# Kernel optimization log

Hardware: AMD Instinct MI355X
Metric: run time of the kernel (lower is better)

## Reference

```python
import jax, jax.numpy as jnp
import numpy as np

B, C, N = 2, 29, 8192
S, K = 1024, 16  # npoint, nsample
D = C + 3


def fps(xyz_t, npoint):
    # xyz_t: [B, N, 3] -> indices [B, npoint] (furthest point sampling, starts at idx 0)
    b, n, _ = xyz_t.shape

    def step(carry, _):
        dists, farthest = carry  # [B,N], [B]
        centroid = jnp.take_along_axis(xyz_t, farthest[:, None, None], axis=1)  # [B,1,3]
        d = jnp.sum((xyz_t - centroid) ** 2, axis=-1)  # [B,N]
        dists = jnp.minimum(dists, d)
        nxt = jnp.argmax(dists, axis=-1)
        return (dists, nxt), farthest

    init = (jnp.full((b, n), 1e10, xyz_t.dtype), jnp.zeros((b,), jnp.int32))
    _, idx = jax.lax.scan(step, init, None, length=npoint)
    return jnp.transpose(idx)  # [B, npoint]


def knn_self(pts, k):
    # pts: [B, S, 3] -> k nearest neighbor indices within the same set, [B, S, k]
    sq = jnp.sum(pts * pts, axis=-1)
    d2 = sq[:, :, None] + sq[:, None, :] - 2.0 * jnp.einsum('bic,bjc->bij', pts, pts)
    _, idx = jax.lax.top_k(-d2, k)
    return idx


def group(arr, idx):
    # arr: [B, C, N], idx: [B, S, K] -> [B, C, S, K]
    return jax.vmap(lambda a, i: a[:, i])(arr, idx)


def squeeze_2x2(x):
    # RealNVP alt-order squeeze: [n, c, h, w] -> [n, 4c, h/2, w/2]
    tl = x[:, :, 0::2, 0::2]
    br = x[:, :, 1::2, 1::2]
    tr = x[:, :, 0::2, 1::2]
    bl = x[:, :, 1::2, 0::2]
    return jnp.concatenate([tl, br, tr, bl], axis=1)


def conv2d(x, w):
    return jax.lax.conv_general_dilated(
        x, w, window_strides=(1, 1), padding='VALID',
        dimension_numbers=('NCHW', 'OIHW', 'NCHW'))


def setup_inputs() -> dict:
    key = jax.random.key(0)
    ks = jax.random.split(key, 6)
    return {
        'xyz': jax.random.normal(ks[0], (B, 3, N), jnp.float32),
        'feats': jax.random.normal(ks[1], (B, C, N), jnp.float32),
        'w0': jax.random.normal(ks[2], (64, 2 * D * 4, 3, 3), jnp.float32) * 0.02,
        'w1': jax.random.normal(ks[3], (64, 64, 3, 3), jnp.float32) * 0.02,
        'w2': jax.random.normal(ks[4], (128, 64, 3, 3), jnp.float32) * 0.02,
        'w3': jax.random.normal(ks[5], (128, 128, 2, 2), jnp.float32) * 0.02,
    }


def reference(xyz, feats, w0, w1, w2, w3):
    b, c, n = feats.shape
    xyz_t = jnp.transpose(xyz, (0, 2, 1))  # [B,N,3]
    fps_idx = fps(xyz_t, S)  # [B,S]
    new_xyz = jnp.take_along_axis(xyz, fps_idx[:, None, :], axis=2)  # [B,3,S]
    new_xyz_t = jnp.transpose(new_xyz, (0, 2, 1))  # [B,S,3]
    idx = knn_self(new_xyz_t, K)  # [B,S,K], values in [0,S)

    pos_grouped = group(new_xyz, idx)  # [B,3,S,K]
    feats_grouped = group(feats, idx)  # [B,C,S,K] (indices < S, as in original)
    pos_diff = pos_grouped - new_xyz[:, :, :, None]
    fg = jnp.concatenate([pos_diff, feats_grouped], axis=1)  # [B,D,S,K]

    # pairwise outer-product features; second half ([fg;1] x [fg;1] upper block) is all ones
    outer = jnp.einsum('bdsi,bdsj->bdsij', fg, fg)  # [B,D,S,K,K]
    mat = jnp.concatenate([outer, jnp.ones_like(outer)], axis=1)  # [B,2D,S,K,K]
    mat = jnp.transpose(mat, (0, 2, 1, 3, 4)).reshape(b * S, 2 * D, K, K)
    mat = squeeze_2x2(mat)  # [B*S, 8D, K/2, K/2]

    for w in (w0, w1, w2, w3):  # use_bn=False -> Identity bns; spatial 8->6->4->2->1
        mat = jax.nn.relu(conv2d(mat, w))

    new_points = jnp.transpose(mat.reshape(b, S, -1), (0, 2, 1))  # [B,128,S]
    return new_xyz, new_points, fps_idx
```

## Files before the change

kernel.cpp:

```cpp
#include <hip/hip_runtime.h>
#include <hip/hip_bf16.h>

#pragma clang fp contract(off)

#define NPTS 8192
#define NS   1024
#define NB   2
#define NC   29
#define NK   16


__global__ __launch_bounds__(256) void prep_kernel(
    const float* __restrict__ w0, const float* __restrict__ w1,
    const float* __restrict__ w2, const float* __restrict__ w3,
    float* __restrict__ w0t, float* __restrict__ w1t,
    float* __restrict__ w2t, float* __restrict__ w3t,
    float* __restrict__ bias0)
{
    int i = blockIdx.x * 256 + threadIdx.x;
    int n = gridDim.x * 256;
    for (int e = i; e < 73728; e += n) {
        int o = e & 63, r = e >> 6, tap = r % 9, ic2 = r / 9;
        int ic = ((ic2 >> 5) << 6) + (ic2 & 31);
        w0t[e] = w0[(o * 256 + ic) * 9 + tap];
    }
    for (int e = i; e < 36864; e += n) {
        int o = e & 63, r = e >> 6, tap = r % 9, ic = r / 9;
        w1t[e] = w1[(o * 64 + ic) * 9 + tap];
    }
    for (int e = i; e < 73728; e += n) {
        int o = e & 127, r = e >> 7, tap = r % 9, ic = r / 9;
        w2t[e] = w2[(o * 64 + ic) * 9 + tap];
    }
    for (int e = i; e < 65536; e += n) {
        int o = e & 127, r = e >> 7, tap = r & 3, ic = r >> 2;
        w3t[e] = w3[(o * 128 + ic) * 4 + tap];
    }
    if (i < 64) {
        float sum = 0.0f;
        for (int q = 0; q < 4; ++q)
            for (int c = 0; c < 32; ++c)
                for (int t = 0; t < 9; ++t)
                    sum += w0[(i * 256 + q * 64 + 32 + c) * 9 + t];
        bias0[i] = sum;
    }
}

__device__ __forceinline__ float wave_max_nonneg(float x) {
    int v = __float_as_int(x);
    int t;
    t = __builtin_amdgcn_update_dpp(0, v, 0x111, 0xf, 0xf, true);
    v = __float_as_int(fmaxf(__int_as_float(v), __int_as_float(t)));
    t = __builtin_amdgcn_update_dpp(0, v, 0x112, 0xf, 0xf, true);
    v = __float_as_int(fmaxf(__int_as_float(v), __int_as_float(t)));
    t = __builtin_amdgcn_update_dpp(0, v, 0x114, 0xf, 0xf, true);
    v = __float_as_int(fmaxf(__int_as_float(v), __int_as_float(t)));
    t = __builtin_amdgcn_update_dpp(0, v, 0x118, 0xf, 0xf, true);
    v = __float_as_int(fmaxf(__int_as_float(v), __int_as_float(t)));
    t = __builtin_amdgcn_update_dpp(0, v, 0x142, 0xa, 0xf, true);
    v = __float_as_int(fmaxf(__int_as_float(v), __int_as_float(t)));
    t = __builtin_amdgcn_update_dpp(0, v, 0x143, 0xc, 0xf, true);
    v = __float_as_int(fmaxf(__int_as_float(v), __int_as_float(t)));
    return __int_as_float(__builtin_amdgcn_readlane(v, 63));
}

__global__ __launch_bounds__(512, 2) void fps_kernel(
    const float* __restrict__ xyz,
    float* __restrict__ nx_ws, float* __restrict__ out)
{
    int b = blockIdx.x;
    int tid = threadIdx.x;
    const float* X = xyz + b * 3 * NPTS;

    __shared__ float s_xyz[3 * NPTS];
    __shared__ unsigned long long s_key[NS];

    float px[16], py[16], pz[16], dist[16];
#pragma unroll
    for (int i = 0; i < 16; ++i) {
        int gi = i * 512 + tid;
        float x = X[gi], y = X[NPTS + gi], z = X[2 * NPTS + gi];
        px[i] = x; py[i] = y; pz[i] = z;
        dist[i] = 1e10f;
        s_xyz[gi] = x; s_xyz[NPTS + gi] = y; s_xyz[2 * NPTS + gi] = z;
    }
    for (int i = tid; i < NS; i += 512) s_key[i] = 0ull;
    if (tid == 0) s_key[0] = 0xFFFFFFFFull;
    __syncthreads();

    float cx = s_xyz[0], cy = s_xyz[NPTS], cz = s_xyz[2 * NPTS];

    for (int it = 1; it < NS; ++it) {
#pragma unroll
        for (int i = 0; i < 16; ++i)
            asm volatile("" : "+v"(px[i]), "+v"(py[i]), "+v"(pz[i]));
#pragma unroll
        for (int i = 0; i < 16; ++i) {
            float dx = px[i] - cx, dy = py[i] - cy, dz = pz[i] - cz;
            float d = (dx * dx + dy * dy) + dz * dz;
            dist[i] = fminf(dist[i], d);
        }
        float t8[8];
#pragma unroll
        for (int i = 0; i < 8; ++i) t8[i] = fmaxf(dist[2 * i], dist[2 * i + 1]);
        float t4[4];
#pragma unroll
        for (int i = 0; i < 4; ++i) t4[i] = fmaxf(t8[2 * i], t8[2 * i + 1]);
        float bv = fmaxf(fmaxf(t4[0], t4[1]), fmaxf(t4[2], t4[3]));
        float wm = wave_max_nonneg(bv);
        if (bv == wm) {
            int gi = 0;
#pragma unroll
            for (int i = 15; i >= 0; --i)
                if (dist[i] == wm) gi = i * 512 + tid;
            unsigned long long key =
                ((unsigned long long)__float_as_uint(wm) << 32) | (unsigned)(~gi);
            atomicMax(&s_key[it], key);
        }
        __syncthreads();
        int idx = (int)(~(unsigned)s_key[it]);
        cx = s_xyz[idx]; cy = s_xyz[NPTS + idx]; cz = s_xyz[2 * NPTS + idx];
    }

    float* out_fps = out + 268288 + b * NS;
    for (int i = tid; i < NS; i += 512) {
        int j = (int)(~(unsigned)s_key[i]);
        out_fps[i] = (float)j;
        float x = s_xyz[j], y = s_xyz[NPTS + j], z = s_xyz[2 * NPTS + j];
        nx_ws[(b * 3 + 0) * NS + i] = x; out[(b * 3 + 0) * NS + i] = x;
        nx_ws[(b * 3 + 1) * NS + i] = y; out[(b * 3 + 1) * NS + i] = y;
        nx_ws[(b * 3 + 2) * NS + i] = z; out[(b * 3 + 2) * NS + i] = z;
    }
}

__global__ __launch_bounds__(256) void knn_kernel(
    const float* __restrict__ nx_ws, int* __restrict__ knn_ws)
{
    int q = blockIdx.x * 4 + (threadIdx.x >> 6);
    int lane = threadIdx.x & 63;
    int b = q >> 10, s = q & 1023;
    const float* P = nx_ws + b * 3 * NS;
    float qx = P[s], qy = P[NS + s], qz = P[2 * NS + s];
    float sqq = (qx * qx + qy * qy) + qz * qz;
    int base_j = lane * 16;
    float d2[16];
    {
        const float4* x4 = (const float4*)(P + base_j);
        const float4* y4 = (const float4*)(P + NS + base_j);
        const float4* z4 = (const float4*)(P + 2 * NS + base_j);
#pragma unroll
        for (int t = 0; t < 4; ++t) {
            float4 xv = x4[t], yv = y4[t], zv = z4[t];
            float xs[4] = { xv.x, xv.y, xv.z, xv.w };
            float ys[4] = { yv.x, yv.y, yv.z, yv.w };
            float zs[4] = { zv.x, zv.y, zv.z, zv.w };
#pragma unroll
            for (int e = 0; e < 4; ++e) {
                float xj = xs[e], yj = ys[e], zj = zs[e];
                float sqj = (xj * xj + yj * yj) + zj * zj;
                float dot = (qx * xj + qy * yj) + qz * zj;
                d2[t * 4 + e] = (sqq + sqj) - 2.0f * dot;
            }
        }
    }
    for (int r = 0; r < NK; ++r) {
        float lv = 3.0e38f; int li = 0;
#pragma unroll
        for (int i = 0; i < 16; ++i) { if (d2[i] < lv) { lv = d2[i]; li = i; } }
        int gj = base_j + li;
#pragma unroll
        for (int off = 32; off > 0; off >>= 1) {
            float ov = __shfl_xor(lv, off, 64);
            int   oj = __shfl_xor(gj, off, 64);
            if (ov < lv || (ov == lv && oj < gj)) { lv = ov; gj = oj; }
        }
        if (lane == 0) knn_ws[q * NK + r] = gj;
        if ((gj >> 4) == lane) {
            int li2 = gj & 15;
#pragma unroll
            for (int i = 0; i < 16; ++i) if (i == li2) d2[i] = 3.0e38f;
        }
    }
}

template<int GODD>
__device__ __forceinline__ void conv0_accum(
    const float* __restrict__ x0r, const float* __restrict__ wbase, float acc[9])
{
    for (int ic2 = 0; ic2 < 128; ++ic2) {
        const float4* x4 = (const float4*)(x0r + ic2 * 64);
        float rr[32];
#pragma unroll
        for (int j = 0; j < 4; ++j) {
            float4 t0 = x4[j * 2], t1 = x4[j * 2 + 1];
            rr[j*8+0]=t0.x; rr[j*8+1]=t0.y; rr[j*8+2]=t0.z; rr[j*8+3]=t0.w;
            rr[j*8+4]=t1.x; rr[j*8+5]=t1.y; rr[j*8+6]=t1.z; rr[j*8+7]=t1.w;
        }
        float w[9];
#pragma unroll
        for (int t = 0; t < 9; ++t) w[t] = wbase[(ic2 * 9 + t) * 64];
#pragma unroll
        for (int pp = 0; pp < 9; ++pp) {
            const int ly = GODD ? (pp < 3 ? 0 : 1) : (pp < 6 ? 0 : 1);
            const int xx = GODD ? (pp < 3 ? pp + 3 : pp - 3) : (pp < 6 ? pp : pp - 6);
#pragma unroll
            for (int ky = 0; ky < 3; ++ky)
#pragma unroll
                for (int kx = 0; kx < 3; ++kx)
                    acc[pp] = __builtin_fmaf(w[ky * 3 + kx], rr[(ly + ky) * 8 + xx + kx], acc[pp]);
        }
    }
}

__global__ __launch_bounds__(256) void conv_kernel(
    const float* __restrict__ feats, const float* __restrict__ nx_ws,
    const int* __restrict__ knn_ws,
    const float* __restrict__ w0t, const float* __restrict__ bias0,
    const float* __restrict__ w1t, const float* __restrict__ w2t,
    const float* __restrict__ w3t, float* __restrict__ out)
{
    __shared__ float s_fg[512];
    __shared__ int   s_ni[16];
    __shared__ float s_x0[8192];
    __shared__ float s_a1[64 * 36];
    __shared__ float s_a2[64 * 16];
    __shared__ float s_a3[128 * 4];

    int bs = blockIdx.x, b = bs >> 10, s = bs & 1023;
    int tid = threadIdx.x;
    if (tid < 16) s_ni[tid] = knn_ws[bs * NK + tid];
    __syncthreads();
    const float* P = nx_ws + b * 3 * NS;
#pragma unroll
    for (int e = tid; e < 512; e += 256) {
        int d = e >> 4, k = e & 15; int j = s_ni[k];
        float v = (d < 3) ? (P[d * NS + j] - P[d * NS + s])
                          : feats[(b * NC + (d - 3)) * NPTS + j];
        s_fg[e] = v;
    }
    __syncthreads();
    for (int e = tid; e < 8192; e += 256) {
        int ic2 = e >> 6, pos = e & 63, u = pos >> 3, v = pos & 7;
        int q = ic2 >> 5, ch = ic2 & 31;
        int ro = q & 1, co = ((q + 1) >> 1) & 1;
        s_x0[e] = s_fg[ch * 16 + 2 * u + ro] * s_fg[ch * 16 + 2 * v + co];
    }
    __syncthreads();

    int o = tid & 63, g = tid >> 6;
    {
        int r0 = g + (g >> 1);
        float acc[9];
        float bz = bias0[o];
#pragma unroll
        for (int p = 0; p < 9; ++p) acc[p] = bz;
        const float* x0r = s_x0 + r0 * 8;
        const float* wb = w0t + o;
        if (g & 1) conv0_accum<1>(x0r, wb, acc);
        else       conv0_accum<0>(x0r, wb, acc);
#pragma unroll
        for (int pp = 0; pp < 9; ++pp) s_a1[o * 36 + g * 9 + pp] = fmaxf(acc[pp], 0.0f);
    }
    __syncthreads();
    {
        float a[4] = {0, 0, 0, 0};
        const float* wb = w1t + o;
        for (int ic = 0; ic < 64; ++ic) {
            const float2* ar2 = (const float2*)(s_a1 + ic * 36 + g * 6);
            float r[18];
#pragma unroll
            for (int t = 0; t < 9; ++t) { float2 tv = ar2[t]; r[t*2] = tv.x; r[t*2+1] = tv.y; }
            float w[9];
#pragma unroll
            for (int t = 0; t < 9; ++t) w[t] = wb[(ic * 9 + t) * 64];
#pragma unroll
            for (int x = 0; x < 4; ++x)
#pragma unroll
                for (int ky = 0; ky < 3; ++ky)
#pragma unroll
                    for (int kx = 0; kx < 3; ++kx)
                        a[x] = __builtin_fmaf(w[ky * 3 + kx], r[ky * 6 + x + kx], a[x]);
        }
#pragma unroll
        for (int x = 0; x < 4; ++x) s_a2[o * 16 + g * 4 + x] = fmaxf(a[x], 0.0f);
    }
    __syncthreads();
    {
        int o2 = tid & 127, g2 = tid >> 7;
        float a[2] = {0, 0};
        const float* wb = w2t + o2;
        for (int ic = 0; ic < 64; ++ic) {
            const float4* ar4 = (const float4*)(s_a2 + ic * 16 + g2 * 4);
            float r[12];
#pragma unroll
            for (int t = 0; t < 3; ++t) { float4 tv = ar4[t]; r[t*4]=tv.x; r[t*4+1]=tv.y; r[t*4+2]=tv.z; r[t*4+3]=tv.w; }
            float w[9];
#pragma unroll
            for (int t = 0; t < 9; ++t) w[t] = wb[(ic * 9 + t) * 128];
#pragma unroll
            for (int x = 0; x < 2; ++x)
#pragma unroll
                for (int ky = 0; ky < 3; ++ky)
#pragma unroll
                    for (int kx = 0; kx < 3; ++kx)
                        a[x] = __builtin_fmaf(w[ky * 3 + kx], r[ky * 4 + x + kx], a[x]);
        }
#pragma unroll
        for (int x = 0; x < 2; ++x) s_a3[o2 * 4 + g2 * 2 + x] = fmaxf(a[x], 0.0f);
    }
    __syncthreads();
    if (tid < 128) {
        float acc = 0.0f;
        const float* wb = w3t + tid;
        for (int ic = 0; ic < 128; ++ic) {
            float4 av = *(const float4*)(s_a3 + ic * 4);
            float wa = wb[(ic * 4 + 0) * 128];
            float wbv = wb[(ic * 4 + 1) * 128];
            float wc = wb[(ic * 4 + 2) * 128];
            float wd = wb[(ic * 4 + 3) * 128];
            acc = __builtin_fmaf(wa, av.x, acc);
            acc = __builtin_fmaf(wbv, av.y, acc);
            acc = __builtin_fmaf(wc, av.z, acc);
            acc = __builtin_fmaf(wd, av.w, acc);
        }
        out[6144 + (b * 128 + tid) * NS + s] = fmaxf(acc, 0.0f);
    }
}

extern "C" void kernel_launch(void* const* d_in, const int* in_sizes, int n_in,
                              void* d_out, int out_size, void* d_ws, size_t ws_size,
                              hipStream_t stream) {
    const float* xyz   = (const float*)d_in[0];
    const float* feats = (const float*)d_in[1];
    const float* w0    = (const float*)d_in[2];
    const float* w1    = (const float*)d_in[3];
    const float* w2    = (const float*)d_in[4];
    const float* w3    = (const float*)d_in[5];
    float* out = (float*)d_out;

    char* ws = (char*)d_ws;
    float* nx_ws  = (float*)(ws + 8192);
    int*   knn_ws = (int*)(ws + 32768);
    float* w0t    = (float*)(ws + 163840);
    float* bias0  = (float*)(ws + 458752);
    float* w1t    = (float*)(ws + 459008);
    float* w2t    = (float*)(ws + 606464);
    float* w3t    = (float*)(ws + 901376);

    prep_kernel<<<128, 256, 0, stream>>>(w0, w1, w2, w3, w0t, w1t, w2t, w3t, bias0);
    fps_kernel<<<NB, 512, 0, stream>>>(xyz, nx_ws, out);
    knn_kernel<<<(NB * NS) / 4, 256, 0, stream>>>(nx_ws, knn_ws);
    conv_kernel<<<NB * NS, 256, 0, stream>>>(feats, nx_ws, knn_ws, w0t, bias0, w1t, w2t, w3t, out);
}
```

Baseline: 1.402 ms.

## Compute outer-product conv0 inputs on the fly instead of staging in LDS

The 8192-float squeezed outer-product tensor is no longer materialised in shared memory. Each thread now recomputes its input rows from the 512-float grouped features inside the conv0 loop, with one template instance per row group. This cuts LDS from about 45KB to about 13KB and removes a barrier, allowing more resident blocks (launch bounds now request 4 per SM), at the cost of extra multiplies and more unrolled code per thread.

After: 1.431 ms. 2.1% more time.

```diff
diff --git a/kernel.cpp b/kernel.cpp
--- a/kernel.cpp
+++ b/kernel.cpp
@@ -183,36 +183,47 @@
     }
 }
 
-template<int GODD>
+template<int G>
 __device__ __forceinline__ void conv0_accum(
-    const float* __restrict__ x0r, const float* __restrict__ wbase, float acc[9])
-{
-    for (int ic2 = 0; ic2 < 128; ++ic2) {
-        const float4* x4 = (const float4*)(x0r + ic2 * 64);
-        float rr[32];
-#pragma unroll
-        for (int j = 0; j < 4; ++j) {
-            float4 t0 = x4[j * 2], t1 = x4[j * 2 + 1];
-            rr[j*8+0]=t0.x; rr[j*8+1]=t0.y; rr[j*8+2]=t0.z; rr[j*8+3]=t0.w;
-            rr[j*8+4]=t1.x; rr[j*8+5]=t1.y; rr[j*8+6]=t1.z; rr[j*8+7]=t1.w;
-        }
-        float w[9];
-#pragma unroll
-        for (int t = 0; t < 9; ++t) w[t] = wbase[(ic2 * 9 + t) * 64];
-#pragma unroll
-        for (int pp = 0; pp < 9; ++pp) {
-            const int ly = GODD ? (pp < 3 ? 0 : 1) : (pp < 6 ? 0 : 1);
-            const int xx = GODD ? (pp < 3 ? pp + 3 : pp - 3) : (pp < 6 ? pp : pp - 6);
-#pragma unroll
-            for (int ky = 0; ky < 3; ++ky)
-#pragma unroll
-                for (int kx = 0; kx < 3; ++kx)
-                    acc[pp] = __builtin_fmaf(w[ky * 3 + kx], rr[(ly + ky) * 8 + xx + kx], acc[pp]);
-        }
-    }
-}
-
-__global__ __launch_bounds__(256) void conv_kernel(
+    const float* __restrict__ s_fg, const float* __restrict__ wbase, float acc[9])
+{
+    constexpr int r0 = G + (G >> 1);
+    constexpr int GODD = G & 1;
+#pragma unroll
+    for (int q = 0; q < 4; ++q) {
+        const int ro = q & 1, co = ((q + 1) >> 1) & 1;
+        const float* wq = wbase + q * 32 * 9 * 64;
+        for (int ch = 0; ch < 32; ++ch) {
+            const float4* f4 = (const float4*)(s_fg + ch * 16);
+            float4 v0 = f4[0], v1 = f4[1], v2 = f4[2], v3 = f4[3];
+            float fg[16] = { v0.x, v0.y, v0.z, v0.w,  v1.x, v1.y, v1.z, v1.w,
+                             v2.x, v2.y, v2.z, v2.w,  v3.x, v3.y, v3.z, v3.w };
+            float rr[32];
+#pragma unroll
+            for (int j = 0; j < 4; ++j) {
+                float aj = fg[2 * (r0 + j) + ro];
+#pragma unroll
+                for (int v = 0; v < 8; ++v)
+                    rr[j * 8 + v] = aj * fg[2 * v + co];
+            }
+            float w[9];
+#pragma unroll
+            for (int t = 0; t < 9; ++t) w[t] = wq[(ch * 9 + t) * 64];
+#pragma unroll
+            for (int pp = 0; pp < 9; ++pp) {
+                const int ly = GODD ? (pp < 3 ? 0 : 1) : (pp < 6 ? 0 : 1);
+                const int xx = GODD ? (pp < 3 ? pp + 3 : pp - 3) : (pp < 6 ? pp : pp - 6);
+#pragma unroll
+                for (int ky = 0; ky < 3; ++ky)
+#pragma unroll
+                    for (int kx = 0; kx < 3; ++kx)
+                        acc[pp] = __builtin_fmaf(w[ky * 3 + kx], rr[(ly + ky) * 8 + xx + kx], acc[pp]);
+            }
+        }
+    }
+}
+
+__global__ __launch_bounds__(256, 4) void conv_kernel(
     const float* __restrict__ feats, const float* __restrict__ nx_ws,
     const int* __restrict__ knn_ws,
     const float* __restrict__ w0t, const float* __restrict__ bias0,
@@ -221,7 +232,6 @@
 {
     __shared__ float s_fg[512];
     __shared__ int   s_ni[16];
-    __shared__ float s_x0[8192];
     __shared__ float s_a1[64 * 36];
     __shared__ float s_a2[64 * 16];
     __shared__ float s_a3[128 * 4];
@@ -239,25 +249,18 @@
         s_fg[e] = v;
     }
     __syncthreads();
-    for (int e = tid; e < 8192; e += 256) {
-        int ic2 = e >> 6, pos = e & 63, u = pos >> 3, v = pos & 7;
-        int q = ic2 >> 5, ch = ic2 & 31;
-        int ro = q & 1, co = ((q + 1) >> 1) & 1;
-        s_x0[e] = s_fg[ch * 16 + 2 * u + ro] * s_fg[ch * 16 + 2 * v + co];
-    }
-    __syncthreads();
 
     int o = tid & 63, g = tid >> 6;
     {
-        int r0 = g + (g >> 1);
         float acc[9];
         float bz = bias0[o];
 #pragma unroll
         for (int p = 0; p < 9; ++p) acc[p] = bz;
-        const float* x0r = s_x0 + r0 * 8;
         const float* wb = w0t + o;
-        if (g & 1) conv0_accum<1>(x0r, wb, acc);
-        else       conv0_accum<0>(x0r, wb, acc);
+        if      (g == 0) conv0_accum<0>(s_fg, wb, acc);
+        else if (g == 1) conv0_accum<1>(s_fg, wb, acc);
+        else if (g == 2) conv0_accum<2>(s_fg, wb, acc);
+        else             conv0_accum<3>(s_fg, wb, acc);
 #pragma unroll
         for (int pp = 0; pp < 9; ++pp) s_a1[o * 36 + g * 9 + pp] = fmaxf(acc[pp], 0.0f);
     }
```
